# Kernel tuning notes

Hardware: AMD Instinct MI355X
Metric: run time of the kernel (lower is better)

## Reference

```python
import jax, jax.numpy as jnp
import numpy as np

N, M = 1024, 32
FN, FE = 64, 32
AGG_N, AGG_E = 128, 64
OUT_N, OUT_E = 64, 32


def _build_indices(n, m):
    nip, eip = [], []
    k = 0
    for i in range(1, n):
        j0 = max(0, i - m)
        nip += list(range(j0, i))
        eip += list(range(k, k + i - j0))
        k += i - j0
    n1 = np.array(nip, np.int32)
    eT = np.array(eip, np.int32)
    n2 = np.concatenate([np.full(min(i, m), i, np.int32) for i in range(1, n)])
    # padded previous-node window indices (0 = zero pad slot)
    prev_nodes = np.zeros(n * m, np.int32)
    k = 0
    for i in range(n):
        t = min(i, m)
        prev_nodes[(i + 1) * m - t:(i + 1) * m] = np.arange(k, k + t) + 1
        k += t
    n_e = k
    norm_node = np.full(n, 1.0 / m, np.float32)
    for i in range(1, m):
        norm_node[i] = 1.0 / i
    prev_edges = np.zeros(n_e * m, np.int32)
    k = 0
    e = 0
    for i in range(n):
        j0 = max(0, i - m)
        for j in range(j0, i):
            if j > j0:
                prev_edges[(e + 1) * m - (j - j0):(e + 1) * m] = np.arange(k, k + j - j0) + 1
            e += 1
        k += i - j0
    norm_edge = np.ones(n_e, np.float32)
    k = 0
    for i in range(1, n):
        t = min(i, m)
        for j in range(t):
            if j > 0:
                norm_edge[k] = 1.0 / j
            k += 1
    return n1, eT, n2, prev_nodes, norm_node, prev_edges, norm_edge, n_e

N1, ET, N2, PREV_N, NORM_N, PREV_E, NORM_E, NE = _build_indices(N, M)
N1 = jnp.asarray(N1); ET = jnp.asarray(ET); N2 = jnp.asarray(N2)
PREV_N = jnp.asarray(PREV_N); PREV_E = jnp.asarray(PREV_E)
NORM_N = jnp.asarray(NORM_N); NORM_E = jnp.asarray(NORM_E)


def setup_inputs() -> dict:
    key = jax.random.key(0)
    ks = jax.random.split(key, 20)
    s = 0.02
    inp = {
        'input_nodes': jax.random.normal(ks[0], (2, N, FN), jnp.float32),
        'input_edges': jax.random.normal(ks[1], (2, NE, FE), jnp.float32),
        # node-branch MLPs (exclude_last=False)
        'Wan1': jax.random.normal(ks[2], (2 * FN + FE, 2 * AGG_N)) * s,
        'ban1': jnp.zeros((2 * AGG_N,)),
        'Wan2': jax.random.normal(ks[3], (2 * AGG_N, AGG_N)) * s,
        'ban2': jnp.zeros((AGG_N,)),
        'Wln1': jax.random.normal(ks[4], (AGG_N + FN, AGG_N + FN)) * s,
        'bln1': jnp.zeros((AGG_N + FN,)),
        'Wln2': jax.random.normal(ks[5], (AGG_N + FN, OUT_N)) * s,
        'bln2': jnp.zeros((OUT_N,)),
        # edge-branch MLPs
        'Wae1': jax.random.normal(ks[6], (FN + FE, 2 * AGG_E)) * s,
        'bae1': jnp.zeros((2 * AGG_E,)),
        'Wae2': jax.random.normal(ks[7], (2 * AGG_E, AGG_E)) * s,
        'bae2': jnp.zeros((AGG_E,)),
        'Wle1': jax.random.normal(ks[8], (AGG_E + FE, AGG_E + FE)) * s,
        'ble1': jnp.zeros((AGG_E + FE,)),
        'Wle2': jax.random.normal(ks[9], (AGG_E + FE, OUT_E)) * s,
        'ble2': jnp.zeros((OUT_E,)),
    }
    return inp


def _mlp2(x, W1, b1, W2, b2):
    return jax.nn.relu(jax.nn.relu(x @ W1 + b1) @ W2 + b2)


def reference(input_nodes, input_edges, Wan1, ban1, Wan2, ban2, Wln1, bln1, Wln2, bln2,
              Wae1, bae1, Wae2, bae2, Wle1, ble1, Wle2, ble2):
    B = input_nodes.shape[0]
    # gather node-edge pairs [B, NE, FN+FE] and node-edge-node triples [B, NE, 2FN+FE]
    pairs = jnp.concatenate([input_nodes[:, N1], input_edges[:, ET]], axis=-1)
    triples = jnp.concatenate([input_nodes[:, N1], input_edges[:, ET], input_nodes[:, N2]], axis=-1)
    # node branch (exclude_last=False -> triples)
    hn = _mlp2(triples, Wan1, ban1, Wan2, ban2)                     # [B, NE, AGG_N]
    hn = jnp.concatenate([jnp.zeros((B, 1, AGG_N), hn.dtype), hn], axis=1)
    pn = hn[:, PREV_N].reshape(B, N, M, AGG_N).sum(axis=2)          # padded window sum
    pn = pn * NORM_N[None, :, None]
    nodes_in = jnp.concatenate([pn, input_nodes], axis=-1)
    out_nodes = _mlp2(nodes_in, Wln1, bln1, Wln2, bln2)             # activation_nodes = relu
    # edge branch (pairs)
    he = _mlp2(pairs, Wae1, bae1, Wae2, bae2)                       # [B, NE, AGG_E]
    he = jnp.concatenate([jnp.zeros((B, 1, AGG_E), he.dtype), he], axis=1)
    pe = he[:, PREV_E].reshape(B, NE, M, AGG_E).sum(axis=2)
    pe = pe * NORM_E[None, :, None]
    edges_in = jnp.concatenate([pe, input_edges], axis=-1)
    out_edges = _mlp2(edges_in, Wle1, ble1, Wle2, ble2)             # activation_edges = relu
    return out_nodes, out_edges
```

## Files before the change

kernel.cpp:

```cpp
#include <hip/hip_runtime.h>
#include <cstdint>

#define NN    1024
#define MM    32
#define NEDGE 32240
#define MROWS 64480
#define PX    168
#define PST   392

typedef unsigned short ushort_t;

typedef __bf16 bf16x8 __attribute__((ext_vector_type(8)));
typedef float  floatx4 __attribute__((ext_vector_type(4)));

__device__ __forceinline__ float b2f(ushort_t u) {
    union { unsigned int i; float f; } v; v.i = ((unsigned int)u) << 16; return v.f;
}
__device__ __forceinline__ ushort_t f2b(float f) {
    unsigned int u = __builtin_bit_cast(unsigned int, f);
    u = (u + 0x7FFFu + ((u >> 16) & 1u)) >> 16;
    return (ushort_t)u;
}
__device__ __forceinline__ int edge_base(int i) {
    return (i <= MM) ? ((i * (i - 1)) >> 1) : (496 + (i - MM) * MM);
}
__device__ __forceinline__ void edge_ij(int e, int& i, int& j) {
    if (e < 496) {
        i = (int)((1.0f + sqrtf(8.0f * (float)e + 1.0f)) * 0.5f);
        while (((i * (i - 1)) >> 1) > e) --i;
        while (((i * (i + 1)) >> 1) <= e) ++i;
        j = e - ((i * (i - 1)) >> 1);
    } else {
        int q = e - 496;
        i = MM + (q >> 5);
        j = i - MM + (q & 31);
    }
}

__global__ __launch_bounds__(256) void k_pack(
        const float* an1, const float* an2, const float* ae1, const float* ae2,
        const float* le1, const float* le2, const float* ln1, const float* ln2,
        const float* nodes, const float* edges,
        ushort_t* pan1, ushort_t* pan2, ushort_t* pae1, ushort_t* pae2,
        ushort_t* ple1, ushort_t* ple2, ushort_t* pln1, ushort_t* pln2,
        ushort_t* nodesb, ushort_t* edgesb, int2* ijt) {
    __shared__ float tile[32][33];
    const int bid = blockIdx.x;
    const int tid = threadIdx.x;
    if (bid < 152) {
        const float* s; ushort_t* d; int K, N, t;
        if (bid < 40)       { s = an1; d = pan1; K = 160; N = 256; t = bid;       }
        else if (bid < 72)  { s = an2; d = pan2; K = 256; N = 128; t = bid - 40;  }
        else if (bid < 84)  { s = ae1; d = pae1; K = 96;  N = 128; t = bid - 72;  }
        else if (bid < 92)  { s = ae2; d = pae2; K = 128; N = 64;  t = bid - 84;  }
        else if (bid < 101) { s = le1; d = ple1; K = 96;  N = 96;  t = bid - 92;  }
        else if (bid < 104) { s = le2; d = ple2; K = 96;  N = 32;  t = bid - 101; }
        else if (bid < 140) { s = ln1; d = pln1; K = 192; N = 192; t = bid - 104; }
        else                { s = ln2; d = pln2; K = 192; N = 64;  t = bid - 140; }
        int ntn = N >> 5;
        int tk = t / ntn, tn = t - tk * ntn;
        int k0 = tk * 32, n0 = tn * 32;
        int tx = tid & 31, ty = tid >> 5;
#pragma unroll
        for (int m = 0; m < 4; ++m)
            tile[ty + m * 8][tx] = s[(size_t)(k0 + ty + m * 8) * N + n0 + tx];
        __syncthreads();
#pragma unroll
        for (int m = 0; m < 4; ++m)
            d[(size_t)(n0 + ty + m * 8) * K + k0 + tx] = f2b(tile[tx][ty + m * 8]);
    } else if (bid < 280) {
        int i4 = (bid - 152) * 256 + tid;
        float4 v = ((const float4*)nodes)[i4];
        uint2 o;
        o.x = (unsigned)f2b(v.x) | ((unsigned)f2b(v.y) << 16);
        o.y = (unsigned)f2b(v.z) | ((unsigned)f2b(v.w) << 16);
        ((uint2*)nodesb)[i4] = o;
    } else if (bid < 2296) {
        int i4 = (bid - 280) * 256 + tid;
        if (i4 < 515840) {
            float4 v = ((const float4*)edges)[i4];
            uint2 o;
            o.x = (unsigned)f2b(v.x) | ((unsigned)f2b(v.y) << 16);
            o.y = (unsigned)f2b(v.z) | ((unsigned)f2b(v.w) << 16);
            ((uint2*)edgesb)[i4] = o;
        }
    } else {
        int e = (bid - 2296) * 256 + tid;
        if (e < NEDGE) { int i, j; edge_ij(e, i, j); ijt[e] = make_int2(i, j); }
    }
}

__global__ __launch_bounds__(512, 2) void k_agg(
        const ushort_t* __restrict__ nodesb, const ushort_t* __restrict__ edgesb,
        const int2* __restrict__ ijt,
        const ushort_t* __restrict__ pan1, const float* __restrict__ ban1,
        const ushort_t* __restrict__ pan2, const float* __restrict__ ban2,
        const ushort_t* __restrict__ pae1, const float* __restrict__ bae1,
        const ushort_t* __restrict__ pae2, const float* __restrict__ bae2,
        ushort_t* __restrict__ hn, ushort_t* __restrict__ he) {
    __shared__ alignas(16) ushort_t X[32 * PX];
    __shared__ alignas(16) ushort_t H[32 * PST];
    const int tid = threadIdx.x;
    const int w = tid >> 6, l = tid & 63, lrow = l & 15, lq = l >> 4;
    const int mt = blockIdx.x;
    floatx4 zero = {0.f, 0.f, 0.f, 0.f};

    bf16x8 B0[5], B1[5], B2[3];
#pragma unroll
    for (int kt = 0; kt < 5; ++kt) {
        B0[kt] = *(const bf16x8*)(pan1 + (size_t)(16 * w + lrow) * 160 + kt * 32 + lq * 8);
        B1[kt] = *(const bf16x8*)(pan1 + (size_t)(16 * (w + 8) + lrow) * 160 + kt * 32 + lq * 8);
    }
#pragma unroll
    for (int kt = 0; kt < 3; ++kt)
        B2[kt] = *(const bf16x8*)(pae1 + (size_t)(16 * w + lrow) * 96 + kt * 32 + lq * 8);
    float c0 = ban1[16 * w + lrow];
    float c1 = ban1[16 * (w + 8) + lrow];
    float c2 = bae1[16 * w + lrow];

#pragma unroll
    for (int k = 0; k < 4; ++k) {
        int rr = w * 4 + k;
        int r = mt * 32 + rr;
        int off = (r >= NEDGE) ? 1 : 0;
        int2 ij = ijt[r - off * NEDGE];
        int bN = off * NN;
        unsigned* xr = (unsigned*)(X + rr * PX);
        const unsigned* nj = (const unsigned*)(nodesb + (size_t)(bN + ij.y) * 64);
        const unsigned* ni = (const unsigned*)(nodesb + (size_t)(bN + ij.x) * 64);
        const unsigned* eb = (const unsigned*)(edgesb + (size_t)r * 32);
        if (l < 32) { xr[l] = nj[l]; xr[48 + l] = ni[l]; }
        else        xr[l] = eb[l - 32];
    }
    __syncthreads();

#pragma unroll
    for (int s = 0; s < 2; ++s) {
        bf16x8 A[5];
#pragma unroll
        for (int kt = 0; kt < 5; ++kt)
            A[kt] = *(const bf16x8*)&X[(s * 16 + lrow) * PX + kt * 32 + lq * 8];
        floatx4 a0 = zero, a1 = zero, a2 = zero;
#pragma unroll
        for (int kt = 0; kt < 5; ++kt) {
            a0 = __builtin_amdgcn_mfma_f32_16x16x32_bf16(A[kt], B0[kt], a0, 0, 0, 0);
            a1 = __builtin_amdgcn_mfma_f32_16x16x32_bf16(A[kt], B1[kt], a1, 0, 0, 0);
        }
#pragma unroll
        for (int kt = 0; kt < 3; ++kt)
            a2 = __builtin_amdgcn_mfma_f32_16x16x32_bf16(A[kt], B2[kt], a2, 0, 0, 0);
#pragma unroll
        for (int r_ = 0; r_ < 4; ++r_) {
            int row = (s * 16 + lq * 4 + r_) * PST;
            H[row + 16 * w + lrow]       = f2b(fmaxf(a0[r_] + c0, 0.f));
            H[row + 128 + 16 * w + lrow] = f2b(fmaxf(a1[r_] + c1, 0.f));
            H[row + 256 + 16 * w + lrow] = f2b(fmaxf(a2[r_] + c2, 0.f));
        }
    }
    __syncthreads();

    floatx4 o0[2], o1[2];
    if (w < 4) {
        bf16x8 D0[8], D1[8];
#pragma unroll
        for (int kt = 0; kt < 8; ++kt) {
            D0[kt] = *(const bf16x8*)(pan2 + (size_t)(16 * w + lrow) * 256 + kt * 32 + lq * 8);
            D1[kt] = *(const bf16x8*)(pan2 + (size_t)(16 * (w + 4) + lrow) * 256 + kt * 32 + lq * 8);
        }
        float d0 = ban2[16 * w + lrow];
        float d1 = ban2[16 * (w + 4) + lrow];
#pragma unroll
        for (int s = 0; s < 2; ++s) {
            floatx4 a0 = zero, a1 = zero;
#pragma unroll
            for (int kt = 0; kt < 8; ++kt) {
                bf16x8 a = *(const bf16x8*)&H[(s * 16 + lrow) * PST + kt * 32 + lq * 8];
                a0 = __builtin_amdgcn_mfma_f32_16x16x32_bf16(a, D0[kt], a0, 0, 0, 0);
                a1 = __builtin_amdgcn_mfma_f32_16x16x32_bf16(a, D1[kt], a1, 0, 0, 0);
            }
#pragma unroll
            for (int r_ = 0; r_ < 4; ++r_) { o0[s][r_] = a0[r_] + d0; o1[s][r_] = a1[r_] + d1; }
        }
    } else {
        int u = w - 4;
        bf16x8 E[4];
#pragma unroll
        for (int kt = 0; kt < 4; ++kt)
            E[kt] = *(const bf16x8*)(pae2 + (size_t)(16 * u + lrow) * 128 + kt * 32 + lq * 8);
        float d2 = bae2[16 * u + lrow];
#pragma unroll
        for (int s = 0; s < 2; ++s) {
            floatx4 a2 = zero;
#pragma unroll
            for (int kt = 0; kt < 4; ++kt) {
                bf16x8 a = *(const bf16x8*)&H[(s * 16 + lrow) * PST + 256 + kt * 32 + lq * 8];
                a2 = __builtin_amdgcn_mfma_f32_16x16x32_bf16(a, E[kt], a2, 0, 0, 0);
            }
#pragma unroll
            for (int r_ = 0; r_ < 4; ++r_) o0[s][r_] = a2[r_] + d2;
        }
    }
    __syncthreads();

    ushort_t* S = X;
    ushort_t* T = H;
    if (w < 4) {
#pragma unroll
        for (int s = 0; s < 2; ++s)
#pragma unroll
            for (int r_ = 0; r_ < 4; ++r_) {
                int row = (s * 16 + lq * 4 + r_) * 136;
                S[row + 16 * w + lrow]        = f2b(fmaxf(o0[s][r_], 0.f));
                S[row + 64 + 16 * w + lrow]   = f2b(fmaxf(o1[s][r_], 0.f));
            }
    } else {
        int u = w - 4;
#pragma unroll
        for (int s = 0; s < 2; ++s)
#pragma unroll
            for (int r_ = 0; r_ < 4; ++r_)
                T[(s * 16 + lq * 4 + r_) * 72 + 16 * u + lrow] = f2b(fmaxf(o0[s][r_], 0.f));
    }
    __syncthreads();

    {
        int row = tid >> 4, c = tid & 15;
        ((uint4*)(hn + (size_t)(mt * 32 + row) * 128))[c] = *(const uint4*)&S[row * 136 + c * 8];
        if (tid < 256) {
            int row2 = tid >> 3, c2 = tid & 7;
            ((uint4*)(he + (size_t)(mt * 32 + row2) * 64))[c2] = *(const uint4*)&T[row2 * 72 + c2 * 8];
        }
    }
}

__global__ __launch_bounds__(256) void k_mid(
        const ushort_t* __restrict__ hn, const ushort_t* __restrict__ he,
        ushort_t* __restrict__ pn, ushort_t* __restrict__ pre) {
    const int tid = threadIdx.x;
    if (blockIdx.x < 2048) {
        int ri = blockIdx.x;
        int b = ri >> 10, i = ri & 1023;
        int t = min(i, MM);
        int base = b * NEDGE + edge_base(i);
        int c = tid & 63, g = tid >> 6;
        float s0 = 0.f, s1 = 0.f;
        for (int p = g; p < t; p += 4) {
            unsigned u = ((const unsigned*)(hn + (size_t)(base + p) * 128))[c];
            s0 += b2f((ushort_t)(u & 0xffff));
            s1 += b2f((ushort_t)(u >> 16));
        }
        __shared__ float red[4][128];
        red[g][c * 2] = s0; red[g][c * 2 + 1] = s1;
        __syncthreads();
        if (tid < 64) {
            float inv = 1.0f / (float)max(t, 1);
            float a0 = (red[0][tid * 2] + red[1][tid * 2] + red[2][tid * 2] + red[3][tid * 2]) * inv;
            float a1 = (red[0][tid * 2 + 1] + red[1][tid * 2 + 1] + red[2][tid * 2 + 1] + red[3][tid * 2 + 1]) * inv;
            ((unsigned*)(pn + (size_t)ri * 128))[tid] = (unsigned)f2b(a0) | ((unsigned)f2b(a1) << 16);
        }
    } else {
        int bi = blockIdx.x - 2048;
        int b = bi >> 10, i = bi & 1023;
        int t = min(i, MM);
        if (t == 0) return;
        int base = b * NEDGE + edge_base(i);
        __shared__ alignas(16) ushort_t hw[32 * 64];
        for (int u = tid; u < t * 8; u += 256)
            ((uint4*)hw)[u] = ((const uint4*)he)[(size_t)base * 8 + u];
        __syncthreads();
        if (tid < 64) {
            float run = 0.f;
            for (int p = 0; p < t; ++p) {
                float v = (p == 0) ? 0.f : run / (float)p;
                pre[(size_t)(base + p) * 64 + tid] = f2b(v);
                run += b2f(hw[p * 64 + tid]);
            }
        }
    }
}

__global__ __launch_bounds__(192) void k_final(
        const ushort_t* __restrict__ pn, const ushort_t* __restrict__ nodesb,
        const ushort_t* __restrict__ pln1, const float* __restrict__ bln1,
        const ushort_t* __restrict__ pln2, const float* __restrict__ bln2,
        float* __restrict__ out_nodes,
        const ushort_t* __restrict__ pre, const ushort_t* __restrict__ edgesb,
        const ushort_t* __restrict__ ple1, const float* __restrict__ ble1,
        const ushort_t* __restrict__ ple2, const float* __restrict__ ble2,
        float* __restrict__ out_edges) {
    __shared__ alignas(16) ushort_t LA[32 * 200];
    __shared__ alignas(16) ushort_t LB[32 * 200];
    const int tid = threadIdx.x;
    const int w = tid >> 6, l = tid & 63, lrow = l & 15, lq = l >> 4;
    floatx4 zero = {0.f, 0.f, 0.f, 0.f};

    if (blockIdx.x < 64) {
        int tile = blockIdx.x;
        for (int u = tid; u < 768; u += 192) {
            int row = u / 24, c = u - row * 24;
            int r = tile * 32 + row;
            const uint4* src = (c < 16) ? ((const uint4*)(pn + (size_t)r * 128) + c)
                                        : ((const uint4*)(nodesb + (size_t)r * 64) + (c - 16));
            *(uint4*)&LA[row * 200 + c * 8] = *src;
        }
        bf16x8 f1[6][4]; float v1[4];
#pragma unroll
        for (int kt = 0; kt < 6; ++kt)
#pragma unroll
            for (int nt = 0; nt < 4; ++nt)
                f1[kt][nt] = *(const bf16x8*)(pln1 + (size_t)(w * 64 + nt * 16 + lrow) * 192 + kt * 32 + lq * 8);
#pragma unroll
        for (int nt = 0; nt < 4; ++nt) v1[nt] = bln1[w * 64 + nt * 16 + lrow];
        __syncthreads();

        floatx4 acc[2][4];
#pragma unroll
        for (int s = 0; s < 2; ++s)
#pragma unroll
            for (int nt = 0; nt < 4; ++nt) acc[s][nt] = zero;
#pragma unroll
        for (int s = 0; s < 2; ++s)
#pragma unroll
            for (int kt = 0; kt < 6; ++kt) {
                bf16x8 a = *(const bf16x8*)&LA[(s * 16 + lrow) * 200 + kt * 32 + lq * 8];
#pragma unroll
                for (int nt = 0; nt < 4; ++nt)
                    acc[s][nt] = __builtin_amdgcn_mfma_f32_16x16x32_bf16(a, f1[kt][nt], acc[s][nt], 0, 0, 0);
            }
#pragma unroll
        for (int s = 0; s < 2; ++s)
#pragma unroll
            for (int nt = 0; nt < 4; ++nt) {
                int col = w * 64 + nt * 16 + lrow;
#pragma unroll
                for (int r_ = 0; r_ < 4; ++r_)
                    LB[(s * 16 + lq * 4 + r_) * 200 + col] = f2b(fmaxf(acc[s][nt][r_] + v1[nt], 0.f));
            }
        bf16x8 f2[6][2]; float v2[2] = {0.f, 0.f};
        if (w < 2) {
#pragma unroll
            for (int kt = 0; kt < 6; ++kt)
#pragma unroll
                for (int nt = 0; nt < 2; ++nt)
                    f2[kt][nt] = *(const bf16x8*)(pln2 + (size_t)(w * 32 + nt * 16 + lrow) * 192 + kt * 32 + lq * 8);
#pragma unroll
            for (int nt = 0; nt < 2; ++nt) v2[nt] = bln2[w * 32 + nt * 16 + lrow];
        }
        __syncthreads();
        if (w < 2) {
            floatx4 a2[2][2];
#pragma unroll
            for (int s = 0; s < 2; ++s) { a2[s][0] = zero; a2[s][1] = zero; }
#pragma unroll
            for (int s = 0; s < 2; ++s)
#pragma unroll
                for (int kt = 0; kt < 6; ++kt) {
                    bf16x8 a = *(const bf16x8*)&LB[(s * 16 + lrow) * 200 + kt * 32 + lq * 8];
#pragma unroll
                    for (int nt = 0; nt < 2; ++nt)
                        a2[s][nt] = __builtin_amdgcn_mfma_f32_16x16x32_bf16(a, f2[kt][nt], a2[s][nt], 0, 0, 0);
                }
#pragma unroll
            for (int s = 0; s < 2; ++s)
#pragma unroll
                for (int nt = 0; nt < 2; ++nt) {
                    int col = w * 32 + nt * 16 + lrow;
#pragma unroll
                    for (int r_ = 0; r_ < 4; ++r_)
                        out_nodes[(size_t)(tile * 32 + s * 16 + lq * 4 + r_) * 64 + col] =
                            fmaxf(a2[s][nt][r_] + v2[nt], 0.f);
                }
        }
    } else {
        int mt = blockIdx.x - 64;
        for (int u = tid; u < 384; u += 192) {
            int row = u / 12, c = u - row * 12;
            int r = mt * 32 + row;
            const uint4* src = (c < 8) ? ((const uint4*)(pre + (size_t)r * 64) + c)
                                       : ((const uint4*)(edgesb + (size_t)r * 32) + (c - 8));
            *(uint4*)&LA[row * 104 + c * 8] = *src;
        }
        bf16x8 fb1[3][2]; float v1[2];
#pragma unroll
        for (int kt = 0; kt < 3; ++kt)
#pragma unroll
            for (int nt = 0; nt < 2; ++nt)
                fb1[kt][nt] = *(const bf16x8*)(ple1 + (size_t)(w * 32 + nt * 16 + lrow) * 96 + kt * 32 + lq * 8);
#pragma unroll
        for (int nt = 0; nt < 2; ++nt) v1[nt] = ble1[w * 32 + nt * 16 + lrow];
        bf16x8 fb2[3]; float v2 = 0.f;
        if (w < 2) {
#pragma unroll
            for (int kt = 0; kt < 3; ++kt)
                fb2[kt] = *(const bf16x8*)(ple2 + (size_t)(w * 16 + lrow) * 96 + kt * 32 + lq * 8);
            v2 = ble2[w * 16 + lrow];
        }
        __syncthreads();

        floatx4 acc[2][2];
#pragma unroll
        for (int s = 0; s < 2; ++s) { acc[s][0] = zero; acc[s][1] = zero; }
#pragma unroll
        for (int s = 0; s < 2; ++s)
#pragma unroll
            for (int kt = 0; kt < 3; ++kt) {
                bf16x8 a = *(const bf16x8*)&LA[(s * 16 + lrow) * 104 + kt * 32 + lq * 8];
#pragma unroll
                for (int nt = 0; nt < 2; ++nt)
                    acc[s][nt] = __builtin_amdgcn_mfma_f32_16x16x32_bf16(a, fb1[kt][nt], acc[s][nt], 0, 0, 0);
            }
#pragma unroll
        for (int s = 0; s < 2; ++s)
#pragma unroll
            for (int nt = 0; nt < 2; ++nt) {
                int col = w * 32 + nt * 16 + lrow;
#pragma unroll
                for (int r_ = 0; r_ < 4; ++r_)
                    LB[(s * 16 + lq * 4 + r_) * 104 + col] = f2b(fmaxf(acc[s][nt][r_] + v1[nt], 0.f));
            }
        __syncthreads();
        if (w < 2) {
            floatx4 a2[2] = {zero, zero};
#pragma unroll
            for (int s = 0; s < 2; ++s)
#pragma unroll
                for (int kt = 0; kt < 3; ++kt) {
                    bf16x8 a = *(const bf16x8*)&LB[(s * 16 + lrow) * 104 + kt * 32 + lq * 8];
                    a2[s] = __builtin_amdgcn_mfma_f32_16x16x32_bf16(a, fb2[kt], a2[s], 0, 0, 0);
                }
#pragma unroll
            for (int s = 0; s < 2; ++s) {
                int col = w * 16 + lrow;
#pragma unroll
                for (int r_ = 0; r_ < 4; ++r_)
                    out_edges[(size_t)(mt * 32 + s * 16 + lq * 4 + r_) * 32 + col] = fmaxf(a2[s][r_] + v2, 0.f);
            }
        }
    }
}

extern "C" void kernel_launch(void* const* d_in, const int* in_sizes, int n_in,
                              void* d_out, int out_size, void* d_ws, size_t ws_size,
                              hipStream_t stream) {
    const float* nodes = (const float*)d_in[0];
    const float* edges = (const float*)d_in[1];
    const float* Wan1 = (const float*)d_in[2];  const float* ban1 = (const float*)d_in[3];
    const float* Wan2 = (const float*)d_in[4];  const float* ban2 = (const float*)d_in[5];
    const float* Wln1 = (const float*)d_in[6];  const float* bln1 = (const float*)d_in[7];
    const float* Wln2 = (const float*)d_in[8];  const float* bln2 = (const float*)d_in[9];
    const float* Wae1 = (const float*)d_in[10]; const float* bae1 = (const float*)d_in[11];
    const float* Wae2 = (const float*)d_in[12]; const float* bae2 = (const float*)d_in[13];
    const float* Wle1 = (const float*)d_in[14]; const float* ble1 = (const float*)d_in[15];
    const float* Wle2 = (const float*)d_in[16]; const float* ble2 = (const float*)d_in[17];

    char* ws = (char*)d_ws;
    size_t o = 0;
    auto alloc = [&](size_t bytes) -> void* {
        void* r = ws + o;
        o += (bytes + 255) & ~(size_t)255;
        return r;
    };
    ushort_t* hn     = (ushort_t*)alloc((size_t)MROWS * 128 * 2);
    ushort_t* he     = (ushort_t*)alloc((size_t)MROWS * 64 * 2);
    ushort_t* pre    = (ushort_t*)alloc((size_t)MROWS * 64 * 2);
    ushort_t* pn     = (ushort_t*)alloc((size_t)2048 * 128 * 2);
    ushort_t* nodesb = (ushort_t*)alloc((size_t)2 * NN * 64 * 2);
    ushort_t* edgesb = (ushort_t*)alloc((size_t)MROWS * 32 * 2);
    int2*     ijt    = (int2*)alloc((size_t)NEDGE * 8);
    ushort_t* pan1 = (ushort_t*)alloc(160 * 256 * 2);
    ushort_t* pan2 = (ushort_t*)alloc(256 * 128 * 2);
    ushort_t* pae1 = (ushort_t*)alloc(96 * 128 * 2);
    ushort_t* pae2 = (ushort_t*)alloc(128 * 64 * 2);
    ushort_t* ple1 = (ushort_t*)alloc(96 * 96 * 2);
    ushort_t* ple2 = (ushort_t*)alloc(96 * 32 * 2);
    ushort_t* pln1 = (ushort_t*)alloc(192 * 192 * 2);
    ushort_t* pln2 = (ushort_t*)alloc(192 * 64 * 2);

    float* out_nodes = (float*)d_out;
    float* out_edges = (float*)d_out + 2 * NN * 64;

    k_pack<<<2422, 256, 0, stream>>>(Wan1, Wan2, Wae1, Wae2, Wle1, Wle2, Wln1, Wln2,
                                     nodes, edges,
                                     pan1, pan2, pae1, pae2, ple1, ple2, pln1, pln2,
                                     nodesb, edgesb, ijt);
    k_agg<<<2015, 512, 0, stream>>>(nodesb, edgesb, ijt,
                                    pan1, ban1, pan2, ban2,
                                    pae1, bae1, pae2, bae2, hn, he);
    k_mid<<<4096, 256, 0, stream>>>(hn, he, pn, pre);
    k_final<<<64 + 2015, 192, 0, stream>>>(pn, nodesb, pln1, bln1, pln2, bln2, out_nodes,
                                           pre, edgesb, ple1, ble1, ple2, ble2, out_edges);

    (void)in_sizes; (void)n_in; (void)out_size; (void)ws_size;
}
```

Measured before the change: 165.1 us.

## Fuse window-sum aggregation kernel into final MLP kernel

Removes the intermediate k_mid kernel and its pn/pre global buffers. The node window sums and the edge prefix means are now computed directly into shared memory inside the final MLP kernel. For the edge tiles, each block loads a halo of up to 31 previous he rows and runs a running prefix sum, using per-row position metadata from ijt. This cuts one launch and a global round trip of the intermediates. In exchange, the prefix loop is serial over 64 threads per block, and the node tiles now gather their sums with only 3 waves.

```diff
diff --git a/kernel.cpp b/kernel.cpp
--- a/kernel.cpp
+++ b/kernel.cpp
@@ -233,75 +233,41 @@
     }
 }
 
-__global__ __launch_bounds__(256) void k_mid(
+__global__ __launch_bounds__(192) void k_fin(
         const ushort_t* __restrict__ hn, const ushort_t* __restrict__ he,
-        ushort_t* __restrict__ pn, ushort_t* __restrict__ pre) {
-    const int tid = threadIdx.x;
-    if (blockIdx.x < 2048) {
-        int ri = blockIdx.x;
-        int b = ri >> 10, i = ri & 1023;
-        int t = min(i, MM);
-        int base = b * NEDGE + edge_base(i);
-        int c = tid & 63, g = tid >> 6;
-        float s0 = 0.f, s1 = 0.f;
-        for (int p = g; p < t; p += 4) {
-            unsigned u = ((const unsigned*)(hn + (size_t)(base + p) * 128))[c];
-            s0 += b2f((ushort_t)(u & 0xffff));
-            s1 += b2f((ushort_t)(u >> 16));
-        }
-        __shared__ float red[4][128];
-        red[g][c * 2] = s0; red[g][c * 2 + 1] = s1;
-        __syncthreads();
-        if (tid < 64) {
-            float inv = 1.0f / (float)max(t, 1);
-            float a0 = (red[0][tid * 2] + red[1][tid * 2] + red[2][tid * 2] + red[3][tid * 2]) * inv;
-            float a1 = (red[0][tid * 2 + 1] + red[1][tid * 2 + 1] + red[2][tid * 2 + 1] + red[3][tid * 2 + 1]) * inv;
-            ((unsigned*)(pn + (size_t)ri * 128))[tid] = (unsigned)f2b(a0) | ((unsigned)f2b(a1) << 16);
-        }
-    } else {
-        int bi = blockIdx.x - 2048;
-        int b = bi >> 10, i = bi & 1023;
-        int t = min(i, MM);
-        if (t == 0) return;
-        int base = b * NEDGE + edge_base(i);
-        __shared__ alignas(16) ushort_t hw[32 * 64];
-        for (int u = tid; u < t * 8; u += 256)
-            ((uint4*)hw)[u] = ((const uint4*)he)[(size_t)base * 8 + u];
-        __syncthreads();
-        if (tid < 64) {
-            float run = 0.f;
-            for (int p = 0; p < t; ++p) {
-                float v = (p == 0) ? 0.f : run / (float)p;
-                pre[(size_t)(base + p) * 64 + tid] = f2b(v);
-                run += b2f(hw[p * 64 + tid]);
-            }
-        }
-    }
-}
-
-__global__ __launch_bounds__(192) void k_final(
-        const ushort_t* __restrict__ pn, const ushort_t* __restrict__ nodesb,
+        const ushort_t* __restrict__ nodesb, const ushort_t* __restrict__ edgesb,
+        const int2* __restrict__ ijt,
         const ushort_t* __restrict__ pln1, const float* __restrict__ bln1,
         const ushort_t* __restrict__ pln2, const float* __restrict__ bln2,
         float* __restrict__ out_nodes,
-        const ushort_t* __restrict__ pre, const ushort_t* __restrict__ edgesb,
         const ushort_t* __restrict__ ple1, const float* __restrict__ ble1,
         const ushort_t* __restrict__ ple2, const float* __restrict__ ble2,
         float* __restrict__ out_edges) {
     __shared__ alignas(16) ushort_t LA[32 * 200];
     __shared__ alignas(16) ushort_t LB[32 * 200];
+    __shared__ int pmeta[32];
     const int tid = threadIdx.x;
     const int w = tid >> 6, l = tid & 63, lrow = l & 15, lq = l >> 4;
     floatx4 zero = {0.f, 0.f, 0.f, 0.f};
 
     if (blockIdx.x < 64) {
         int tile = blockIdx.x;
-        for (int u = tid; u < 768; u += 192) {
-            int row = u / 24, c = u - row * 24;
-            int r = tile * 32 + row;
-            const uint4* src = (c < 16) ? ((const uint4*)(pn + (size_t)r * 128) + c)
-                                        : ((const uint4*)(nodesb + (size_t)r * 64) + (c - 16));
-            *(uint4*)&LA[row * 200 + c * 8] = *src;
+        for (int n = w; n < 32; n += 3) {
+            int ri = tile * 32 + n;
+            int b = ri >> 10, i = ri & 1023;
+            int t = min(i, MM);
+            int base = b * NEDGE + edge_base(i);
+            const unsigned* hp = (const unsigned*)(hn + (size_t)base * 128) + l;
+            float s0 = 0.f, s1 = 0.f;
+            for (int p = 0; p < t; ++p) {
+                unsigned u = hp[(size_t)p * 64];
+                s0 += b2f((ushort_t)(u & 0xffff));
+                s1 += b2f((ushort_t)(u >> 16));
+            }
+            float inv = 1.0f / (float)max(t, 1);
+            ((unsigned*)&LA[n * 200])[l] = (unsigned)f2b(s0 * inv) | ((unsigned)f2b(s1 * inv) << 16);
+            if (l < 32)
+                ((unsigned*)&LA[n * 200 + 128])[l] = ((const unsigned*)(nodesb + (size_t)ri * 64))[l];
         }
         bf16x8 f1[6][4]; float v1[4];
 #pragma unroll
@@ -367,18 +333,27 @@
                     int col = w * 32 + nt * 16 + lrow;
 #pragma unroll
                     for (int r_ = 0; r_ < 4; ++r_)
-                        out_nodes[(size_t)(tile * 32 + s * 16 + lq * 4 + r_) * 64 + col] =
+                        out_nodes[(size_t)(blockIdx.x * 32 + s * 16 + lq * 4 + r_) * 64 + col] =
                             fmaxf(a2[s][nt][r_] + v2[nt], 0.f);
                 }
         }
     } else {
         int mt = blockIdx.x - 64;
-        for (int u = tid; u < 384; u += 192) {
-            int row = u / 12, c = u - row * 12;
-            int r = mt * 32 + row;
-            const uint4* src = (c < 8) ? ((const uint4*)(pre + (size_t)r * 64) + c)
-                                       : ((const uint4*)(edgesb + (size_t)r * 32) + (c - 8));
-            *(uint4*)&LA[row * 104 + c * 8] = *src;
+        int r0 = mt * 32;
+        int lo = max(r0 - 31, 0);
+        int nrows = r0 + 32 - lo;
+        ushort_t* HW = LB;
+        for (int u = tid; u < nrows * 8; u += 192)
+            ((uint4*)HW)[u] = ((const uint4*)(he + (size_t)lo * 64))[u];
+        if (tid < 32) {
+            int r = r0 + tid;
+            int off = (r >= NEDGE) ? 1 : 0;
+            int e = r - off * NEDGE;
+            pmeta[tid] = e - edge_base(ijt[e].x);
+        }
+        for (int u = tid; u < 128; u += 192) {
+            int row = u >> 2, c = u & 3;
+            *(uint4*)&LA[row * 104 + 64 + c * 8] = ((const uint4*)(edgesb + (size_t)(r0 + row) * 32))[c];
         }
         bf16x8 fb1[3][2]; float v1[2];
 #pragma unroll
@@ -397,6 +372,22 @@
         }
         __syncthreads();
 
+        if (tid < 64) {
+            int c = tid;
+            int p0 = pmeta[0];
+            float run = 0.f;
+            for (int q = r0 - p0 - lo; q < r0 - lo; ++q) run += b2f(HW[q * 64 + c]);
+            for (int k = 0; k < 32; ++k) {
+                int p = pmeta[k];
+                float v;
+                if (p == 0) { run = 0.f; v = 0.f; }
+                else v = run / (float)p;
+                LA[k * 104 + c] = f2b(v);
+                run += b2f(HW[(r0 + k - lo) * 64 + c]);
+            }
+        }
+        __syncthreads();
+
         floatx4 acc[2][2];
 #pragma unroll
         for (int s = 0; s < 2; ++s) { acc[s][0] = zero; acc[s][1] = zero; }
@@ -409,6 +400,7 @@
                 for (int nt = 0; nt < 2; ++nt)
                     acc[s][nt] = __builtin_amdgcn_mfma_f32_16x16x32_bf16(a, fb1[kt][nt], acc[s][nt], 0, 0, 0);
             }
+        __syncthreads();
 #pragma unroll
         for (int s = 0; s < 2; ++s)
 #pragma unroll
@@ -462,8 +454,6 @@
     };
     ushort_t* hn     = (ushort_t*)alloc((size_t)MROWS * 128 * 2);
     ushort_t* he     = (ushort_t*)alloc((size_t)MROWS * 64 * 2);
-    ushort_t* pre    = (ushort_t*)alloc((size_t)MROWS * 64 * 2);
-    ushort_t* pn     = (ushort_t*)alloc((size_t)2048 * 128 * 2);
     ushort_t* nodesb = (ushort_t*)alloc((size_t)2 * NN * 64 * 2);
     ushort_t* edgesb = (ushort_t*)alloc((size_t)MROWS * 32 * 2);
     int2*     ijt    = (int2*)alloc((size_t)NEDGE * 8);
@@ -486,9 +476,9 @@
     k_agg<<<2015, 512, 0, stream>>>(nodesb, edgesb, ijt,
                                     pan1, ban1, pan2, ban2,
                                     pae1, bae1, pae2, bae2, hn, he);
-    k_mid<<<4096, 256, 0, stream>>>(hn, he, pn, pre);
-    k_final<<<64 + 2015, 192, 0, stream>>>(pn, nodesb, pln1, bln1, pln2, bln2, out_nodes,
-                                           pre, edgesb, ple1, ble1, ple2, ble2, out_edges);
+    k_fin<<<64 + 2015, 192, 0, stream>>>(hn, he, nodesb, edgesb, ijt,
+                                         pln1, bln1, pln2, bln2, out_nodes,
+                                         ple1, ble1, ple2, ble2, out_edges);
 
     (void)in_sizes; (void)n_in; (void)out_size; (void)ws_size;
 }
```

Measured after the change: 253.5 us. +53.6%, slower.
